# Optimization experiments

Measured on AMD Instinct MI355X. Metric: run time of the kernel, lower is better.

The kernel has to match this reference:

```python
import jax, jax.numpy as jnp
import numpy as np

EPS = 1e-5

def channel_norm(x):
    # per-(batch,channel) norm over spatial dims; torch.var default is unbiased (ddof=1)
    mn = x.mean(axis=(-1, -2), keepdims=True)
    std = jnp.sqrt(x.var(axis=(-1, -2), keepdims=True, ddof=1) + EPS)
    return (x - mn) / std

def conv1x1(x, W, b):
    # x: [B,C,H,W], W: [O,C], b: [O]
    return jnp.einsum('oc,bchw->bohw', W, x) + b[None, :, None, None]

def setup_inputs() -> dict:
    key = jax.random.key(0)
    ks = jax.random.split(key, 10)
    B, C, H, W = 4, 512, 64, 64
    s = 1.0 / np.sqrt(C)  # kaiming-uniform-ish scale for 1x1 conv
    inp = {
        'f_c': jax.random.normal(ks[0], (B, C, H, W), jnp.float32),
        'f_s': jax.random.normal(ks[1], (B, C, H, W), jnp.float32),
        'W_c1': jax.random.uniform(ks[2], (C, C), jnp.float32, -s, s),
        'b_c1': jax.random.uniform(ks[3], (C,), jnp.float32, -s, s),
        'W_s1': jax.random.uniform(ks[4], (C, C), jnp.float32, -s, s),
        'b_s1': jax.random.uniform(ks[5], (C,), jnp.float32, -s, s),
        'W_s2': jax.random.uniform(ks[6], (C, C), jnp.float32, -s, s),
        'b_s2': jax.random.uniform(ks[7], (C,), jnp.float32, -s, s),
        'W_csc': jax.random.uniform(ks[8], (C, C), jnp.float32, -s, s),
        'b_csc': jax.random.uniform(ks[9], (C,), jnp.float32, -s, s),
    }
    return inp

def reference(f_c, f_s, W_c1, b_c1, W_s1, b_s1, W_s2, b_s2, W_csc, b_csc):
    B, C, H, W = f_c.shape
    f_c_hat = channel_norm(f_c)
    f_s_hat = channel_norm(f_s)
    f = conv1x1(f_c_hat, W_c1, b_c1).reshape(B, C, H * W)  # queries [B,C,N]
    g = conv1x1(f_s_hat, W_s1, b_s1).reshape(B, C, H * W)  # keys    [B,C,N]
    scores = jnp.einsum('bci,bcj->bij', f, g)              # [B,N,N]
    attention = jax.nn.softmax(scores, axis=-1)
    h = conv1x1(f_s_hat, W_s2, b_s2).reshape(B, C, H * W)  # values  [B,C,N]
    out = jnp.einsum('bcj,bij->bci', h, attention).reshape(B, C, H, W)
    return conv1x1(out, W_csc, b_csc) + f_c
```

## Files before the change

kernel.cpp:

```cpp
#include <hip/hip_runtime.h>

typedef unsigned short u16;
typedef __attribute__((ext_vector_type(8))) _Float16 f16x8;
typedef __attribute__((ext_vector_type(4))) float f32x4;

#define N_SP 4096
#define C_CH 512
#define B_SZ 4

struct PtrTab { u16* p[4]; };

__device__ __forceinline__ u16 f2h(float f) {
    union { _Float16 h; u16 u; } x; x.h = (_Float16)f; return x.u;
}
__device__ __forceinline__ float h2f(u16 u) {
    union { u16 u; _Float16 h; } x; x.u = u; return (float)x.h;
}
__device__ __forceinline__ void async_cp16(const void* g, void* l) {
    __builtin_amdgcn_global_load_lds((const __attribute__((address_space(1))) unsigned*)g,
                                     (__attribute__((address_space(3))) unsigned*)l, 16, 0, 0);
}
__device__ __forceinline__ float wave_reduce_sum(float v) {
    #pragma unroll
    for (int off = 32; off; off >>= 1) v += __shfl_xor(v, off, 64);
    return v;
}
__device__ __forceinline__ float wave_reduce_max(float v) {
    #pragma unroll
    for (int off = 32; off; off >>= 1) v = fmaxf(v, __shfl_xor(v, off, 64));
    return v;
}

__global__ __launch_bounds__(256) void transpose_cast_stats(
        const float* __restrict__ fc, const float* __restrict__ fs,
        u16* __restrict__ xc, u16* __restrict__ xs,
        float* __restrict__ part_s, float* __restrict__ part_ss) {
    __shared__ float tile[64][65];
    const int t = threadIdx.x;
    const int n0 = blockIdx.x * 64, c0 = blockIdx.y * 64;
    const int z = blockIdx.z;
    const int b = z & 3, which = z >> 2;
    const float* src = which ? fs : fc;
    u16* dst = which ? xs : xc;
    const int r = t >> 4, q4 = (t & 15) * 4;
    #pragma unroll
    for (int it = 0; it < 4; ++it) {
        const int row = it * 16 + r;
        float4 v = *(const float4*)(src + ((size_t)b * C_CH + c0 + row) * N_SP + n0 + q4);
        tile[row][q4 + 0] = v.x; tile[row][q4 + 1] = v.y;
        tile[row][q4 + 2] = v.z; tile[row][q4 + 3] = v.w;
    }
    __syncthreads();
    {
        const int cr = t >> 2, q = t & 3;
        float s = 0.f, ss = 0.f;
        #pragma unroll
        for (int i = 0; i < 16; ++i) {
            float a = tile[cr][q * 16 + i];
            s += a; ss += a * a;
        }
        s += __shfl_xor(s, 1, 64);  s += __shfl_xor(s, 2, 64);
        ss += __shfl_xor(ss, 1, 64); ss += __shfl_xor(ss, 2, 64);
        if (q == 0) {
            atomicAdd(&part_s[z * 512 + c0 + cr], s);
            atomicAdd(&part_ss[z * 512 + c0 + cr], ss);
        }
    }
    #pragma unroll
    for (int it = 0; it < 4; ++it) {
        const int nrow = it * 16 + r;
        ushort4 h4;
        h4.x = f2h(tile[q4 + 0][nrow]);
        h4.y = f2h(tile[q4 + 1][nrow]);
        h4.z = f2h(tile[q4 + 2][nrow]);
        h4.w = f2h(tile[q4 + 3][nrow]);
        *(ushort4*)(dst + ((size_t)b * N_SP + n0 + nrow) * C_CH + c0 + q4) = h4;
    }
}

__global__ __launch_bounds__(256) void finalize_stats(const float* __restrict__ part_s,
                                                      const float* __restrict__ part_ss,
                                                      float* __restrict__ mu_a,
                                                      float* __restrict__ rs_a) {
    const int wb = blockIdx.x, t = threadIdx.x;
    #pragma unroll
    for (int h = 0; h < 2; ++h) {
        const int c = wb * 512 + h * 256 + t;
        const float S = part_s[c], SS = part_ss[c];
        const float mean = S * (1.f / N_SP);
        const float var = (SS - S * mean) * (1.f / (N_SP - 1));
        mu_a[c] = mean;
        rs_a[c] = rsqrtf(var + 1e-5f);
    }
}

__global__ __launch_bounds__(256) void wtrans(const float* __restrict__ W0, const float* __restrict__ W1,
                                              const float* __restrict__ W2, const float* __restrict__ W3,
                                              u16* __restrict__ D0, u16* __restrict__ D1,
                                              u16* __restrict__ D2, u16* __restrict__ D3) {
    __shared__ float tile[64][65];
    const int t = threadIdx.x, z = blockIdx.z;
    const int n0 = blockIdx.x * 64, c0 = blockIdx.y * 64;
    const float* W = (z == 0) ? W0 : (z == 1) ? W1 : (z == 2) ? W2 : W3;
    u16* D = (z == 0) ? D0 : (z == 1) ? D1 : (z == 2) ? D2 : D3;
    const int r = t >> 4, q4 = (t & 15) * 4;
    #pragma unroll
    for (int it = 0; it < 4; ++it) {
        const int row = it * 16 + r;
        float4 v = *(const float4*)(W + (size_t)(c0 + row) * 512 + n0 + q4);
        if (z == 3) {
            ushort4 h4 = { f2h(v.x), f2h(v.y), f2h(v.z), f2h(v.w) };
            *(ushort4*)(D + (size_t)(c0 + row) * 512 + n0 + q4) = h4;
        } else {
            tile[row][q4 + 0] = v.x; tile[row][q4 + 1] = v.y;
            tile[row][q4 + 2] = v.z; tile[row][q4 + 3] = v.w;
        }
    }
    __syncthreads();
    if (z == 3) return;
    #pragma unroll
    for (int it = 0; it < 4; ++it) {
        const int nrow = it * 16 + r;
        ushort4 h4;
        h4.x = f2h(tile[q4 + 0][nrow]);
        h4.y = f2h(tile[q4 + 1][nrow]);
        h4.z = f2h(tile[q4 + 2][nrow]);
        h4.w = f2h(tile[q4 + 3][nrow]);
        *(ushort4*)(D + (size_t)(n0 + nrow) * 512 + c0 + q4) = h4;
    }
}

__global__ __launch_bounds__(256) void wu_gemv(const float* __restrict__ Ws1,
                                               const float* __restrict__ bc1,
                                               float* __restrict__ w_u) {
    const int d = blockIdx.x * 256 + threadIdx.x;
    float acc = 0.f;
    for (int o = 0; o < 512; ++o) acc += bc1[o] * Ws1[(size_t)o * 512 + d];
    w_u[d] = acc;
}

__global__ __launch_bounds__(256) void bfold_gemv(const float* __restrict__ Wcsc,
                                                  const float* __restrict__ bs2,
                                                  const float* __restrict__ bcsc,
                                                  float* __restrict__ bfold0) {
    const int o = blockIdx.x * 4 + (threadIdx.x >> 6), l = threadIdx.x & 63;
    const float4 w0 = *(const float4*)(Wcsc + (size_t)o * 512 + l * 8);
    const float4 w1 = *(const float4*)(Wcsc + (size_t)o * 512 + l * 8 + 4);
    const float4 b0 = *(const float4*)(bs2 + l * 8);
    const float4 b1 = *(const float4*)(bs2 + l * 8 + 4);
    float acc = w0.x * b0.x + w0.y * b0.y + w0.z * b0.z + w0.w * b0.w
              + w1.x * b1.x + w1.y * b1.y + w1.z * b1.z + w1.w * b1.w;
    acc = wave_reduce_sum(acc);
    if (l == 0) bfold0[o] = acc + bcsc[o];
}

__global__ __launch_bounds__(256) void make_scaled(const u16* __restrict__ WqT16,
                                                   const u16* __restrict__ Wf16,
                                                   const float* __restrict__ rs_a,
                                                   u16* __restrict__ Wq_z, u16* __restrict__ Wf_z) {
    const int y = blockIdx.y;
    const size_t e = ((size_t)blockIdx.x * 256 + threadIdx.x) * 8;
    const int z = (int)(e >> 18), rem = (int)(e & 262143);
    const int d = rem >> 9, a0 = rem & 511;
    u16 v[8];
    if (y == 0) {
        *(uint4*)v = *(const uint4*)(WqT16 + rem);
        const float rd = rs_a[(4 + z) * 512 + d];
        const float* rc = rs_a + z * 512 + a0;
        #pragma unroll
        for (int i = 0; i < 8; ++i) v[i] = f2h(h2f(v[i]) * rc[i] * rd);
        *(uint4*)(Wq_z + e) = *(const uint4*)v;
    } else {
        *(uint4*)v = *(const uint4*)(Wf16 + rem);
        const float* rk = rs_a + (4 + z) * 512 + a0;
        #pragma unroll
        for (int i = 0; i < 8; ++i) v[i] = f2h(h2f(v[i]) * rk[i]);
        *(uint4*)(Wf_z + e) = *(const uint4*)v;
    }
}

__global__ __launch_bounds__(256) void bias2_gemv(const u16* __restrict__ WqT16,
                                                  const u16* __restrict__ Wf16,
                                                  const float* __restrict__ mu_a,
                                                  const float* __restrict__ rs_a,
                                                  const float* __restrict__ bfold0,
                                                  float* __restrict__ bq, float* __restrict__ bh) {
    const int w = threadIdx.x >> 6, l = threadIdx.x & 63;
    const int oid = blockIdx.x * 4 + w;
    const int kind = oid >> 11;
    const int z = (oid >> 9) & 3, d = oid & 511;
    const u16* row = (kind == 0 ? WqT16 : Wf16) + (size_t)d * 512;
    const int sb = (kind == 0 ? z : 4 + z) * 512;
    float acc = 0.f;
    #pragma unroll
    for (int i = 0; i < 8; ++i) {
        const int a = l * 8 + i;
        acc += h2f(row[a]) * mu_a[sb + a] * rs_a[sb + a];
    }
    acc = wave_reduce_sum(acc);
    if (l == 0) {
        if (kind == 0) bq[z * 512 + d] = -acc * rs_a[(4 + z) * 512 + d];
        else           bh[z * 512 + d] = bfold0[d] - acc;
    }
}

__global__ __launch_bounds__(256) void u_big(const u16* __restrict__ xs,
                                             const float* __restrict__ w_u,
                                             const float* __restrict__ rs_a,
                                             float* __restrict__ u) {
    const int b = blockIdx.y, w = threadIdx.x >> 6, l = threadIdx.x & 63;
    float4 u0 = *(const float4*)(w_u + l * 8);
    float4 u1 = *(const float4*)(w_u + l * 8 + 4);
    const float4 r0 = *(const float4*)(rs_a + (4 + b) * 512 + l * 8);
    const float4 r1 = *(const float4*)(rs_a + (4 + b) * 512 + l * 8 + 4);
    u0.x *= r0.x; u0.y *= r0.y; u0.z *= r0.z; u0.w *= r0.w;
    u1.x *= r1.x; u1.y *= r1.y; u1.z *= r1.z; u1.w *= r1.w;
    #pragma unroll
    for (int jj = 0; jj < 16; ++jj) {
        const int j = blockIdx.x * 64 + w * 16 + jj;
        const u16* row = xs + ((size_t)b * N_SP + j) * C_CH + l * 8;
        f16x8 x = *(const f16x8*)row;
        float acc = (float)x[0] * u0.x + (float)x[1] * u0.y + (float)x[2] * u0.z + (float)x[3] * u0.w
                  + (float)x[4] * u1.x + (float)x[5] * u1.y + (float)x[6] * u1.z + (float)x[7] * u1.w;
        acc = wave_reduce_sum(acc);
        if (l == 0) u[(size_t)b * N_SP + j] = acc;
    }
}

enum { OUT_F32 = 0, OUT_F16 = 1 };

template<int OUTMODE, bool TABB, bool TABD>
__global__ __launch_bounds__(256) void gemm_bt(
    const u16* __restrict__ A, const u16* __restrict__ B, PtrTab tab,
    float* __restrict__ Df, u16* __restrict__ Dh,
    const float* __restrict__ bias_m, const float* __restrict__ bias_n,
    const float* __restrict__ res,
    int M, int N, int K, int lda, int ldb, int ldd,
    size_t sA, size_t sB, size_t sD, size_t sR, int sBm, int sBn)
{
    constexpr int TM = 128, TN = 128, BK = 64;
    __shared__ u16 smem[(TM + TN) * BK];
    u16* As = smem;
    u16* Bs = smem + TM * BK;

    const int t = threadIdx.x;
    const int l = t & 63, w = t >> 6;
    const int m0 = blockIdx.y * TM, n0 = blockIdx.x * TN;
    const size_t zb = blockIdx.z;
    const u16* pA = A + zb * sA + (size_t)m0 * lda;
    const u16* pB = (TABB ? tab.p[zb] : B + zb * sB) + (size_t)n0 * ldb;

    const int wr = (w & 1) * 64, wc = (w >> 1) * 64;

    f32x4 acc[4][4] = {};

    for (int k0 = 0; k0 < K; k0 += BK) {
        #pragma unroll
        for (int it = 0; it < 4; ++it) {
            const int L = it * 256 + t;
            const int row = L >> 3, c = L & 7;
            const int sc = (c ^ (row & 7)) * 8;
            async_cp16(pA + (size_t)row * lda + k0 + sc, As + L * 8);
        }
        #pragma unroll
        for (int it = 0; it < 4; ++it) {
            const int L = it * 256 + t;
            const int row = L >> 3, c = L & 7;
            const int sc = (c ^ (row & 7)) * 8;
            async_cp16(pB + (size_t)row * ldb + k0 + sc, Bs + L * 8);
        }
        __syncthreads();
        #pragma unroll
        for (int kk = 0; kk < 2; ++kk) {
            const int cc = (l >> 4) + kk * 4;
            f16x8 af[4], bf[4];
            #pragma unroll
            for (int i = 0; i < 4; ++i) {
                const int row = wr + i * 16 + (l & 15);
                af[i] = *(const f16x8*)(As + row * BK + ((cc ^ (row & 7)) * 8));
            }
            #pragma unroll
            for (int j = 0; j < 4; ++j) {
                const int row = wc + j * 16 + (l & 15);
                bf[j] = *(const f16x8*)(Bs + row * BK + ((cc ^ (row & 7)) * 8));
            }
            #pragma unroll
            for (int i = 0; i < 4; ++i)
                #pragma unroll
                for (int j = 0; j < 4; ++j)
                    acc[i][j] = __builtin_amdgcn_mfma_f32_16x16x32_f16(af[i], bf[j], acc[i][j], 0, 0, 0);
        }
        __syncthreads();
    }

    const int em = m0 + wr + (l >> 4) * 4;
    const int en = n0 + wc + (l & 15);
    u16* pDh = (OUTMODE == OUT_F16) ? (TABD ? tab.p[zb] : Dh + zb * sD) : nullptr;
    float* pDf = (OUTMODE == OUT_F32) ? (Df + zb * sD) : nullptr;
    #pragma unroll
    for (int i = 0; i < 4; ++i) {
        #pragma unroll
        for (int j = 0; j < 4; ++j) {
            const int nn = en + j * 16;
            const float bn = bias_n ? bias_n[(size_t)sBn * zb + nn] : 0.f;
            #pragma unroll
            for (int r = 0; r < 4; ++r) {
                const int mm = em + i * 16 + r;
                float v = acc[i][j][r] + bn;
                if (bias_m) v += bias_m[(size_t)sBm * zb + mm];
                const size_t off = (size_t)mm * ldd + nn;
                if (OUTMODE == OUT_F32) {
                    if (res) v += res[zb * sR + off];
                    pDf[off] = v;
                } else {
                    pDh[off] = f2h(v);
                }
            }
        }
    }
}

__global__ __launch_bounds__(256) void softmax_kernel(PtrTab tab) {
    u16* row = tab.p[blockIdx.y] + (size_t)blockIdx.x * N_SP;
    const int t = threadIdx.x;
    u16 raw[16];
    *(uint4*)(raw + 0) = *(const uint4*)(row + t * 16);
    *(uint4*)(raw + 8) = *(const uint4*)(row + t * 16 + 8);
    float v[16];
    float mx = -1e30f;
    #pragma unroll
    for (int i = 0; i < 16; ++i) { v[i] = h2f(raw[i]); mx = fmaxf(mx, v[i]); }
    mx = wave_reduce_max(mx);
    __shared__ float red[4];
    const int wave = t >> 6;
    if ((t & 63) == 0) red[wave] = mx;
    __syncthreads();
    mx = fmaxf(fmaxf(red[0], red[1]), fmaxf(red[2], red[3]));
    float sum = 0.f;
    #pragma unroll
    for (int i = 0; i < 16; ++i) { v[i] = __expf(v[i] - mx); sum += v[i]; }
    sum = wave_reduce_sum(sum);
    __syncthreads();
    if ((t & 63) == 0) red[wave] = sum;
    __syncthreads();
    const float inv = 1.f / (red[0] + red[1] + red[2] + red[3]);
    #pragma unroll
    for (int i = 0; i < 16; ++i) raw[i] = f2h(v[i] * inv);
    *(uint4*)(row + t * 16)     = *(const uint4*)(raw + 0);
    *(uint4*)(row + t * 16 + 8) = *(const uint4*)(raw + 8);
}

extern "C" void kernel_launch(void* const* d_in, const int* in_sizes, int n_in,
                              void* d_out, int out_size, void* d_ws, size_t ws_size,
                              hipStream_t stream) {
    const float* f_c   = (const float*)d_in[0];
    const float* f_s   = (const float*)d_in[1];
    const float* W_c1  = (const float*)d_in[2];
    const float* b_c1  = (const float*)d_in[3];
    const float* W_s1  = (const float*)d_in[4];
    const float* b_s1  = (const float*)d_in[5]; (void)b_s1;
    const float* W_s2  = (const float*)d_in[6];
    const float* b_s2  = (const float*)d_in[7];
    const float* W_csc = (const float*)d_in[8];
    const float* b_csc = (const float*)d_in[9];

    const size_t PB = (size_t)N_SP * C_CH;
    const size_t M1 = 1024 * 1024;

    u16* ws   = (u16*)d_ws;
    u16* Xs   = ws;
    u16* q_   = ws + 8 * M1;
    u16* hc   = ws + 16 * M1;
    u16* Xc   = ws + 24 * M1;
    u16* S3   = ws + 24 * M1;
    u16* S0   = ws + 40 * M1;
    u16* S1   = ws + 56 * M1;
    u16* S2   = ws + 72 * M1;
    u16* Wc1T = ws + 88 * M1;
    u16* Ws1T = Wc1T + 262144;
    u16* Ws2T = Ws1T + 262144;
    u16* Wcs16= Ws2T + 262144;
    u16* WqT16= Wcs16 + 262144;
    u16* Wf16 = WqT16 + 262144;
    u16* Wq_z = Wf16 + 262144;
    u16* Wf_z = Wq_z + 1048576;
    float* f32b = (float*)(ws + 92 * M1);
    float* part_s  = f32b;
    float* part_ss = f32b + 4096;
    float* mu_a    = f32b + 8192;
    float* rs_a    = f32b + 12288;
    float* w_u     = f32b + 16384;
    float* bfold0  = f32b + 16896;
    float* bq      = f32b + 17408;
    float* bh      = f32b + 19456;
    float* u_      = f32b + 21504;

    PtrTab Stab; Stab.p[0] = S0; Stab.p[1] = S1; Stab.p[2] = S2; Stab.p[3] = S3;
    PtrTab tab0 = Stab;

    hipMemsetAsync(part_s, 0, 2 * 4096 * sizeof(float), stream);

    transpose_cast_stats<<<dim3(64, 8, 8), 256, 0, stream>>>(f_c, f_s, Xc, Xs, part_s, part_ss);
    finalize_stats<<<8, 256, 0, stream>>>(part_s, part_ss, mu_a, rs_a);
    wtrans<<<dim3(8, 8, 4), 256, 0, stream>>>(W_c1, W_s1, W_s2, W_csc, Wc1T, Ws1T, Ws2T, Wcs16);
    wu_gemv<<<2, 256, 0, stream>>>(W_s1, b_c1, w_u);
    bfold_gemv<<<128, 256, 0, stream>>>(W_csc, b_s2, b_csc, bfold0);

    gemm_bt<OUT_F16, false, false><<<dim3(4, 4, 1), 256, 0, stream>>>(
        Ws1T, Wc1T, tab0, nullptr, WqT16, nullptr, nullptr, nullptr,
        512, 512, 512, 512, 512, 512, 0, 0, 0, 0, 0, 0);
    gemm_bt<OUT_F16, false, false><<<dim3(4, 4, 1), 256, 0, stream>>>(
        Wcs16, Ws2T, tab0, nullptr, Wf16, nullptr, nullptr, nullptr,
        512, 512, 512, 512, 512, 512, 0, 0, 0, 0, 0, 0);

    make_scaled<<<dim3(512, 2), 256, 0, stream>>>(WqT16, Wf16, rs_a, Wq_z, Wf_z);
    bias2_gemv<<<1024, 256, 0, stream>>>(WqT16, Wf16, mu_a, rs_a, bfold0, bq, bh);

    gemm_bt<OUT_F16, false, false><<<dim3(4, 32, B_SZ), 256, 0, stream>>>(
        Xc, Wq_z, tab0, nullptr, q_, nullptr, bq, nullptr,
        N_SP, C_CH, C_CH, C_CH, C_CH, C_CH, PB, 262144, PB, 0, 0, 512);
    gemm_bt<OUT_F16, false, false><<<dim3(32, 4, B_SZ), 256, 0, stream>>>(
        Wf_z, Xs, tab0, nullptr, hc, bh, nullptr, nullptr,
        C_CH, N_SP, C_CH, C_CH, C_CH, N_SP, 262144, PB, PB, 0, 512, 0);
    u_big<<<dim3(64, B_SZ), 256, 0, stream>>>(Xs, w_u, rs_a, u_);

    gemm_bt<OUT_F16, false, true><<<dim3(32, 32, B_SZ), 256, 0, stream>>>(
        q_, Xs, Stab, nullptr, nullptr, nullptr, u_, nullptr,
        N_SP, N_SP, C_CH, C_CH, C_CH, N_SP, PB, PB, 0, 0, 0, N_SP);

    softmax_kernel<<<dim3(N_SP, B_SZ), 256, 0, stream>>>(Stab);

    gemm_bt<OUT_F32, true, false><<<dim3(32, 4, B_SZ), 256, 0, stream>>>(
        hc, nullptr, Stab, (float*)d_out, nullptr, nullptr, nullptr, f_c,
        C_CH, N_SP, N_SP, N_SP, N_SP, N_SP, PB, 0, PB, PB, 0, 0);
}
```

Baseline: 476.2 us.

## Merge prep kernels into fewer launches and switch GEMM to 32x32x16 MFMA

Merges finalize_stats, wtrans, wu_gemv and bfold_gemv into one prep1 kernel, and make_scaled, bias2_gemv and u_big into one prep2 kernel. The two small weight-product GEMMs are batched into one launch by laying the weight buffers out contiguously. The main GEMM inner loop moves from 16x16x32 MFMA tiles to 32x32x16 MFMA with a 2x2 accumulator layout and a matching epilogue index mapping. This cuts launch overhead and may raise MFMA throughput in the large score and output GEMMs, at the cost of riskier register use and a changed LDS read pattern.

```diff
diff --git a/kernel.cpp b/kernel.cpp
--- a/kernel.cpp
+++ b/kernel.cpp
@@ -2,7 +2,7 @@
 
 typedef unsigned short u16;
 typedef __attribute__((ext_vector_type(8))) _Float16 f16x8;
-typedef __attribute__((ext_vector_type(4))) float f32x4;
+typedef __attribute__((ext_vector_type(16))) float f32x16;
 
 #define N_SP 4096
 #define C_CH 512
@@ -78,152 +78,147 @@
     }
 }
 
-__global__ __launch_bounds__(256) void finalize_stats(const float* __restrict__ part_s,
-                                                      const float* __restrict__ part_ss,
-                                                      float* __restrict__ mu_a,
-                                                      float* __restrict__ rs_a) {
-    const int wb = blockIdx.x, t = threadIdx.x;
-    #pragma unroll
-    for (int h = 0; h < 2; ++h) {
-        const int c = wb * 512 + h * 256 + t;
-        const float S = part_s[c], SS = part_ss[c];
-        const float mean = S * (1.f / N_SP);
-        const float var = (SS - S * mean) * (1.f / (N_SP - 1));
-        mu_a[c] = mean;
-        rs_a[c] = rsqrtf(var + 1e-5f);
-    }
-}
-
-__global__ __launch_bounds__(256) void wtrans(const float* __restrict__ W0, const float* __restrict__ W1,
-                                              const float* __restrict__ W2, const float* __restrict__ W3,
-                                              u16* __restrict__ D0, u16* __restrict__ D1,
-                                              u16* __restrict__ D2, u16* __restrict__ D3) {
+__global__ __launch_bounds__(256) void prep1(
+        const float* __restrict__ W_c1, const float* __restrict__ W_s1,
+        const float* __restrict__ W_s2, const float* __restrict__ W_csc,
+        const float* __restrict__ b_c1, const float* __restrict__ b_s2,
+        const float* __restrict__ b_csc,
+        u16* __restrict__ Wbase,
+        const float* __restrict__ part_s, const float* __restrict__ part_ss,
+        float* __restrict__ mu_a, float* __restrict__ rs_a,
+        float* __restrict__ w_u, float* __restrict__ bfold0) {
     __shared__ float tile[64][65];
     const int t = threadIdx.x, z = blockIdx.z;
-    const int n0 = blockIdx.x * 64, c0 = blockIdx.y * 64;
-    const float* W = (z == 0) ? W0 : (z == 1) ? W1 : (z == 2) ? W2 : W3;
-    u16* D = (z == 0) ? D0 : (z == 1) ? D1 : (z == 2) ? D2 : D3;
-    const int r = t >> 4, q4 = (t & 15) * 4;
-    #pragma unroll
-    for (int it = 0; it < 4; ++it) {
-        const int row = it * 16 + r;
-        float4 v = *(const float4*)(W + (size_t)(c0 + row) * 512 + n0 + q4);
-        if (z == 3) {
-            ushort4 h4 = { f2h(v.x), f2h(v.y), f2h(v.z), f2h(v.w) };
-            *(ushort4*)(D + (size_t)(c0 + row) * 512 + n0 + q4) = h4;
+    if (z < 4) {
+        const int n0 = blockIdx.x * 64, c0 = blockIdx.y * 64;
+        const float* W = (z == 0) ? W_c1 : (z == 1) ? W_s1 : (z == 2) ? W_s2 : W_csc;
+        u16* D = Wbase + ((z == 0) ? 2 : (z == 1) ? 0 : (z == 2) ? 3 : 1) * 262144;
+        const int r = t >> 4, q4 = (t & 15) * 4;
+        #pragma unroll
+        for (int it = 0; it < 4; ++it) {
+            const int row = it * 16 + r;
+            float4 v = *(const float4*)(W + (size_t)(c0 + row) * 512 + n0 + q4);
+            if (z == 3) {
+                ushort4 h4 = { f2h(v.x), f2h(v.y), f2h(v.z), f2h(v.w) };
+                *(ushort4*)(D + (size_t)(c0 + row) * 512 + n0 + q4) = h4;
+            } else {
+                tile[row][q4 + 0] = v.x; tile[row][q4 + 1] = v.y;
+                tile[row][q4 + 2] = v.z; tile[row][q4 + 3] = v.w;
+            }
+        }
+        __syncthreads();
+        if (z == 3) return;
+        #pragma unroll
+        for (int it = 0; it < 4; ++it) {
+            const int nrow = it * 16 + r;
+            ushort4 h4;
+            h4.x = f2h(tile[q4 + 0][nrow]);
+            h4.y = f2h(tile[q4 + 1][nrow]);
+            h4.z = f2h(tile[q4 + 2][nrow]);
+            h4.w = f2h(tile[q4 + 3][nrow]);
+            *(ushort4*)(D + (size_t)(n0 + nrow) * 512 + c0 + q4) = h4;
+        }
+        return;
+    }
+    const int flat = blockIdx.y * 8 + blockIdx.x;
+    if (flat < 8) {
+        #pragma unroll
+        for (int h = 0; h < 2; ++h) {
+            const int c = flat * 512 + h * 256 + t;
+            const float S = part_s[c], SS = part_ss[c];
+            const float mean = S * (1.f / N_SP);
+            const float var = (SS - S * mean) * (1.f / (N_SP - 1));
+            mu_a[c] = mean;
+            rs_a[c] = rsqrtf(var + 1e-5f);
+        }
+    } else if (flat < 10) {
+        const int d = (flat - 8) * 256 + t;
+        float acc = 0.f;
+        for (int o = 0; o < 512; ++o) acc += b_c1[o] * W_s1[(size_t)o * 512 + d];
+        w_u[d] = acc;
+    } else if (flat < 42) {
+        const int w4 = t >> 6, l = t & 63;
+        #pragma unroll
+        for (int q = 0; q < 4; ++q) {
+            const int o = (flat - 10) * 16 + w4 * 4 + q;
+            const float4 w0 = *(const float4*)(W_csc + (size_t)o * 512 + l * 8);
+            const float4 w1 = *(const float4*)(W_csc + (size_t)o * 512 + l * 8 + 4);
+            const float4 b0 = *(const float4*)(b_s2 + l * 8);
+            const float4 b1 = *(const float4*)(b_s2 + l * 8 + 4);
+            float acc = w0.x * b0.x + w0.y * b0.y + w0.z * b0.z + w0.w * b0.w
+                      + w1.x * b1.x + w1.y * b1.y + w1.z * b1.z + w1.w * b1.w;
+            acc = wave_reduce_sum(acc);
+            if (l == 0) bfold0[o] = acc + b_csc[o];
+        }
+    }
+}
+
+__global__ __launch_bounds__(256) void prep2(
+        const u16* __restrict__ WqT16, const u16* __restrict__ Wf16,
+        const u16* __restrict__ xs,
+        const float* __restrict__ mu_a, const float* __restrict__ rs_a,
+        const float* __restrict__ bfold0, const float* __restrict__ w_u,
+        u16* __restrict__ Wq_z, u16* __restrict__ Wf_z,
+        float* __restrict__ bq, float* __restrict__ bh, float* __restrict__ u_) {
+    const int id = blockIdx.x, t = threadIdx.x;
+    if (id < 1024) {
+        const int y = id >> 9;
+        const size_t e = ((size_t)(id & 511) * 256 + t) * 8;
+        const int z = (int)(e >> 18), rem = (int)(e & 262143);
+        const int d = rem >> 9, a0 = rem & 511;
+        u16 v[8];
+        if (y == 0) {
+            *(uint4*)v = *(const uint4*)(WqT16 + rem);
+            const float rd = rs_a[(4 + z) * 512 + d];
+            const float* rc = rs_a + z * 512 + a0;
+            #pragma unroll
+            for (int i = 0; i < 8; ++i) v[i] = f2h(h2f(v[i]) * rc[i] * rd);
+            *(uint4*)(Wq_z + e) = *(const uint4*)v;
         } else {
-            tile[row][q4 + 0] = v.x; tile[row][q4 + 1] = v.y;
-            tile[row][q4 + 2] = v.z; tile[row][q4 + 3] = v.w;
-        }
-    }
-    __syncthreads();
-    if (z == 3) return;
-    #pragma unroll
-    for (int it = 0; it < 4; ++it) {
-        const int nrow = it * 16 + r;
-        ushort4 h4;
-        h4.x = f2h(tile[q4 + 0][nrow]);
-        h4.y = f2h(tile[q4 + 1][nrow]);
-        h4.z = f2h(tile[q4 + 2][nrow]);
-        h4.w = f2h(tile[q4 + 3][nrow]);
-        *(ushort4*)(D + (size_t)(n0 + nrow) * 512 + c0 + q4) = h4;
-    }
-}
-
-__global__ __launch_bounds__(256) void wu_gemv(const float* __restrict__ Ws1,
-                                               const float* __restrict__ bc1,
-                                               float* __restrict__ w_u) {
-    const int d = blockIdx.x * 256 + threadIdx.x;
-    float acc = 0.f;
-    for (int o = 0; o < 512; ++o) acc += bc1[o] * Ws1[(size_t)o * 512 + d];
-    w_u[d] = acc;
-}
-
-__global__ __launch_bounds__(256) void bfold_gemv(const float* __restrict__ Wcsc,
-                                                  const float* __restrict__ bs2,
-                                                  const float* __restrict__ bcsc,
-                                                  float* __restrict__ bfold0) {
-    const int o = blockIdx.x * 4 + (threadIdx.x >> 6), l = threadIdx.x & 63;
-    const float4 w0 = *(const float4*)(Wcsc + (size_t)o * 512 + l * 8);
-    const float4 w1 = *(const float4*)(Wcsc + (size_t)o * 512 + l * 8 + 4);
-    const float4 b0 = *(const float4*)(bs2 + l * 8);
-    const float4 b1 = *(const float4*)(bs2 + l * 8 + 4);
-    float acc = w0.x * b0.x + w0.y * b0.y + w0.z * b0.z + w0.w * b0.w
-              + w1.x * b1.x + w1.y * b1.y + w1.z * b1.z + w1.w * b1.w;
-    acc = wave_reduce_sum(acc);
-    if (l == 0) bfold0[o] = acc + bcsc[o];
-}
-
-__global__ __launch_bounds__(256) void make_scaled(const u16* __restrict__ WqT16,
-                                                   const u16* __restrict__ Wf16,
-                                                   const float* __restrict__ rs_a,
-                                                   u16* __restrict__ Wq_z, u16* __restrict__ Wf_z) {
-    const int y = blockIdx.y;
-    const size_t e = ((size_t)blockIdx.x * 256 + threadIdx.x) * 8;
-    const int z = (int)(e >> 18), rem = (int)(e & 262143);
-    const int d = rem >> 9, a0 = rem & 511;
-    u16 v[8];
-    if (y == 0) {
-        *(uint4*)v = *(const uint4*)(WqT16 + rem);
-        const float rd = rs_a[(4 + z) * 512 + d];
-        const float* rc = rs_a + z * 512 + a0;
-        #pragma unroll
-        for (int i = 0; i < 8; ++i) v[i] = f2h(h2f(v[i]) * rc[i] * rd);
-        *(uint4*)(Wq_z + e) = *(const uint4*)v;
+            *(uint4*)v = *(const uint4*)(Wf16 + rem);
+            const float* rk = rs_a + (4 + z) * 512 + a0;
+            #pragma unroll
+            for (int i = 0; i < 8; ++i) v[i] = f2h(h2f(v[i]) * rk[i]);
+            *(uint4*)(Wf_z + e) = *(const uint4*)v;
+        }
+    } else if (id < 2048) {
+        const int w = t >> 6, l = t & 63;
+        const int oid = (id - 1024) * 4 + w;
+        const int kind = oid >> 11;
+        const int z = (oid >> 9) & 3, d = oid & 511;
+        const u16* row = (kind == 0 ? WqT16 : Wf16) + (size_t)d * 512;
+        const int sb = (kind == 0 ? z : 4 + z) * 512;
+        float acc = 0.f;
+        #pragma unroll
+        for (int i = 0; i < 8; ++i) {
+            const int a = l * 8 + i;
+            acc += h2f(row[a]) * mu_a[sb + a] * rs_a[sb + a];
+        }
+        acc = wave_reduce_sum(acc);
+        if (l == 0) {
+            if (kind == 0) bq[z * 512 + d] = -acc * rs_a[(4 + z) * 512 + d];
+            else           bh[z * 512 + d] = bfold0[d] - acc;
+        }
     } else {
-        *(uint4*)v = *(const uint4*)(Wf16 + rem);
-        const float* rk = rs_a + (4 + z) * 512 + a0;
-        #pragma unroll
-        for (int i = 0; i < 8; ++i) v[i] = f2h(h2f(v[i]) * rk[i]);
-        *(uint4*)(Wf_z + e) = *(const uint4*)v;
-    }
-}
-
-__global__ __launch_bounds__(256) void bias2_gemv(const u16* __restrict__ WqT16,
-                                                  const u16* __restrict__ Wf16,
-                                                  const float* __restrict__ mu_a,
-                                                  const float* __restrict__ rs_a,
-                                                  const float* __restrict__ bfold0,
-                                                  float* __restrict__ bq, float* __restrict__ bh) {
-    const int w = threadIdx.x >> 6, l = threadIdx.x & 63;
-    const int oid = blockIdx.x * 4 + w;
-    const int kind = oid >> 11;
-    const int z = (oid >> 9) & 3, d = oid & 511;
-    const u16* row = (kind == 0 ? WqT16 : Wf16) + (size_t)d * 512;
-    const int sb = (kind == 0 ? z : 4 + z) * 512;
-    float acc = 0.f;
-    #pragma unroll
-    for (int i = 0; i < 8; ++i) {
-        const int a = l * 8 + i;
-        acc += h2f(row[a]) * mu_a[sb + a] * rs_a[sb + a];
-    }
-    acc = wave_reduce_sum(acc);
-    if (l == 0) {
-        if (kind == 0) bq[z * 512 + d] = -acc * rs_a[(4 + z) * 512 + d];
-        else           bh[z * 512 + d] = bfold0[d] - acc;
-    }
-}
-
-__global__ __launch_bounds__(256) void u_big(const u16* __restrict__ xs,
-                                             const float* __restrict__ w_u,
-                                             const float* __restrict__ rs_a,
-                                             float* __restrict__ u) {
-    const int b = blockIdx.y, w = threadIdx.x >> 6, l = threadIdx.x & 63;
-    float4 u0 = *(const float4*)(w_u + l * 8);
-    float4 u1 = *(const float4*)(w_u + l * 8 + 4);
-    const float4 r0 = *(const float4*)(rs_a + (4 + b) * 512 + l * 8);
-    const float4 r1 = *(const float4*)(rs_a + (4 + b) * 512 + l * 8 + 4);
-    u0.x *= r0.x; u0.y *= r0.y; u0.z *= r0.z; u0.w *= r0.w;
-    u1.x *= r1.x; u1.y *= r1.y; u1.z *= r1.z; u1.w *= r1.w;
-    #pragma unroll
-    for (int jj = 0; jj < 16; ++jj) {
-        const int j = blockIdx.x * 64 + w * 16 + jj;
-        const u16* row = xs + ((size_t)b * N_SP + j) * C_CH + l * 8;
-        f16x8 x = *(const f16x8*)row;
-        float acc = (float)x[0] * u0.x + (float)x[1] * u0.y + (float)x[2] * u0.z + (float)x[3] * u0.w
-                  + (float)x[4] * u1.x + (float)x[5] * u1.y + (float)x[6] * u1.z + (float)x[7] * u1.w;
-        acc = wave_reduce_sum(acc);
-        if (l == 0) u[(size_t)b * N_SP + j] = acc;
+        const int id2 = id - 2048;
+        const int b = id2 >> 6, xblk = id2 & 63;
+        const int w = t >> 6, l = t & 63;
+        float4 u0 = *(const float4*)(w_u + l * 8);
+        float4 u1 = *(const float4*)(w_u + l * 8 + 4);
+        const float4 r0 = *(const float4*)(rs_a + (4 + b) * 512 + l * 8);
+        const float4 r1 = *(const float4*)(rs_a + (4 + b) * 512 + l * 8 + 4);
+        u0.x *= r0.x; u0.y *= r0.y; u0.z *= r0.z; u0.w *= r0.w;
+        u1.x *= r1.x; u1.y *= r1.y; u1.z *= r1.z; u1.w *= r1.w;
+        #pragma unroll
+        for (int jj = 0; jj < 16; ++jj) {
+            const int j = xblk * 64 + w * 16 + jj;
+            const u16* row = xs + ((size_t)b * N_SP + j) * C_CH + l * 8;
+            f16x8 x = *(const f16x8*)row;
+            float acc = (float)x[0] * u0.x + (float)x[1] * u0.y + (float)x[2] * u0.z + (float)x[3] * u0.w
+                      + (float)x[4] * u1.x + (float)x[5] * u1.y + (float)x[6] * u1.z + (float)x[7] * u1.w;
+            acc = wave_reduce_sum(acc);
+            if (l == 0) u_[(size_t)b * N_SP + j] = acc;
+        }
     }
 }
 
@@ -252,7 +247,7 @@
 
     const int wr = (w & 1) * 64, wc = (w >> 1) * 64;
 
-    f32x4 acc[4][4] = {};
+    f32x16 acc[2][2] = {};
 
     for (int k0 = 0; k0 < K; k0 += BK) {
         #pragma unroll
@@ -271,42 +266,43 @@
         }
         __syncthreads();
         #pragma unroll
-        for (int kk = 0; kk < 2; ++kk) {
-            const int cc = (l >> 4) + kk * 4;
-            f16x8 af[4], bf[4];
-            #pragma unroll
-            for (int i = 0; i < 4; ++i) {
-                const int row = wr + i * 16 + (l & 15);
-                af[i] = *(const f16x8*)(As + row * BK + ((cc ^ (row & 7)) * 8));
+        for (int kk = 0; kk < 4; ++kk) {
+            f16x8 af[2], bf[2];
+            #pragma unroll
+            for (int i = 0; i < 2; ++i) {
+                const int row = wr + i * 32 + (l & 31);
+                const int ch = ((kk * 2 + (l >> 5)) ^ (row & 7)) * 8;
+                af[i] = *(const f16x8*)(As + row * BK + ch);
             }
             #pragma unroll
-            for (int j = 0; j < 4; ++j) {
-                const int row = wc + j * 16 + (l & 15);
-                bf[j] = *(const f16x8*)(Bs + row * BK + ((cc ^ (row & 7)) * 8));
+            for (int j = 0; j < 2; ++j) {
+                const int row = wc + j * 32 + (l & 31);
+                const int ch = ((kk * 2 + (l >> 5)) ^ (row & 7)) * 8;
+                bf[j] = *(const f16x8*)(Bs + row * BK + ch);
             }
             #pragma unroll
-            for (int i = 0; i < 4; ++i)
+            for (int i = 0; i < 2; ++i)
                 #pragma unroll
-                for (int j = 0; j < 4; ++j)
-                    acc[i][j] = __builtin_amdgcn_mfma_f32_16x16x32_f16(af[i], bf[j], acc[i][j], 0, 0, 0);
+                for (int j = 0; j < 2; ++j)
+                    acc[i][j] = __builtin_amdgcn_mfma_f32_32x32x16_f16(af[i], bf[j], acc[i][j], 0, 0, 0);
         }
         __syncthreads();
     }
 
-    const int em = m0 + wr + (l >> 4) * 4;
-    const int en = n0 + wc + (l & 15);
+    const int cl = l & 31, rh = (l >> 5) * 4;
     u16* pDh = (OUTMODE == OUT_F16) ? (TABD ? tab.p[zb] : Dh + zb * sD) : nullptr;
     float* pDf = (OUTMODE == OUT_F32) ? (Df + zb * sD) : nullptr;
     #pragma unroll
-    for (int i = 0; i < 4; ++i) {
-        #pragma unroll
-        for (int j = 0; j < 4; ++j) {
-            const int nn = en + j * 16;
+    for (int i = 0; i < 2; ++i) {
+        #pragma unroll
+        for (int j = 0; j < 2; ++j) {
+            const int nn = n0 + wc + j * 32 + cl;
             const float bn = bias_n ? bias_n[(size_t)sBn * zb + nn] : 0.f;
             #pragma unroll
-            for (int r = 0; r < 4; ++r) {
-                const int mm = em + i * 16 + r;
-                float v = acc[i][j][r] + bn;
+            for (int reg = 0; reg < 16; ++reg) {
+                const int ml = (reg & 3) + 8 * (reg >> 2) + rh;
+                const int mm = m0 + wr + i * 32 + ml;
+                float v = acc[i][j][reg] + bn;
                 if (bias_m) v += bias_m[(size_t)sBm * zb + mm];
                 const size_t off = (size_t)mm * ldd + nn;
                 if (OUTMODE == OUT_F32) {
@@ -376,13 +372,10 @@
     u16* S0   = ws + 40 * M1;
     u16* S1   = ws + 56 * M1;
     u16* S2   = ws + 72 * M1;
-    u16* Wc1T = ws + 88 * M1;
-    u16* Ws1T = Wc1T + 262144;
-    u16* Ws2T = Ws1T + 262144;
-    u16* Wcs16= Ws2T + 262144;
-    u16* WqT16= Wcs16 + 262144;
-    u16* Wf16 = WqT16 + 262144;
-    u16* Wq_z = Wf16 + 262144;
+    u16* Wbase= ws + 88 * M1;
+    u16* WqT16= Wbase + 4 * 262144;
+    u16* Wf16 = Wbase + 5 * 262144;
+    u16* Wq_z = Wbase + 6 * 262144;
     u16* Wf_z = Wq_z + 1048576;
     float* f32b = (float*)(ws + 92 * M1);
     float* part_s  = f32b;
@@ -401,20 +394,16 @@
     hipMemsetAsync(part_s, 0, 2 * 4096 * sizeof(float), stream);
 
     transpose_cast_stats<<<dim3(64, 8, 8), 256, 0, stream>>>(f_c, f_s, Xc, Xs, part_s, part_ss);
-    finalize_stats<<<8, 256, 0, stream>>>(part_s, part_ss, mu_a, rs_a);
-    wtrans<<<dim3(8, 8, 4), 256, 0, stream>>>(W_c1, W_s1, W_s2, W_csc, Wc1T, Ws1T, Ws2T, Wcs16);
-    wu_gemv<<<2, 256, 0, stream>>>(W_s1, b_c1, w_u);
-    bfold_gemv<<<128, 256, 0, stream>>>(W_csc, b_s2, b_csc, bfold0);
-
-    gemm_bt<OUT_F16, false, false><<<dim3(4, 4, 1), 256, 0, stream>>>(
-        Ws1T, Wc1T, tab0, nullptr, WqT16, nullptr, nullptr, nullptr,
-        512, 512, 512, 512, 512, 512, 0, 0, 0, 0, 0, 0);
-    gemm_bt<OUT_F16, false, false><<<dim3(4, 4, 1), 256, 0, stream>>>(
-        Wcs16, Ws2T, tab0, nullptr, Wf16, nullptr, nullptr, nullptr,
-        512, 512, 512, 512, 512, 512, 0, 0, 0, 0, 0, 0);
-
-    make_scaled<<<dim3(512, 2), 256, 0, stream>>>(WqT16, Wf16, rs_a, Wq_z, Wf_z);
-    bias2_gemv<<<1024, 256, 0, stream>>>(WqT16, Wf16, mu_a, rs_a, bfold0, bq, bh);
+
+    prep1<<<dim3(8, 8, 5), 256, 0, stream>>>(W_c1, W_s1, W_s2, W_csc, b_c1, b_s2, b_csc,
+                                             Wbase, part_s, part_ss, mu_a, rs_a, w_u, bfold0);
+
+    gemm_bt<OUT_F16, false, false><<<dim3(4, 4, 2), 256, 0, stream>>>(
+        Wbase, Wbase + 2 * 262144, tab0, nullptr, WqT16, nullptr, nullptr, nullptr,
+        512, 512, 512, 512, 512, 512, 262144, 262144, 262144, 0, 0, 0);
+
+    prep2<<<2304, 256, 0, stream>>>(WqT16, Wf16, Xs, mu_a, rs_a, bfold0, w_u,
+                                    Wq_z, Wf_z, bq, bh, u_);
 
     gemm_bt<OUT_F16, false, false><<<dim3(4, 32, B_SZ), 256, 0, stream>>>(
         Xc, Wq_z, tab0, nullptr, q_, nullptr, bq, nullptr,
@@ -422,7 +411,6 @@
     gemm_bt<OUT_F16, false, false><<<dim3(32, 4, B_SZ), 256, 0, stream>>>(
         Wf_z, Xs, tab0, nullptr, hc, bh, nullptr, nullptr,
         C_CH, N_SP, C_CH, C_CH, C_CH, N_SP, 262144, PB, PB, 0, 512, 0);
-    u_big<<<dim3(64, B_SZ), 256, 0, stream>>>(Xs, w_u, rs_a, u_);
 
     gemm_bt<OUT_F16, false, true><<<dim3(32, 32, B_SZ), 256, 0, stream>>>(
         q_, Xs, Stab, nullptr, nullptr, nullptr, u_, nullptr,
```

Result: faster. 450.8 us (-5.3%).
